# Kernel tuning notes

Hardware: AMD Instinct MI355X
Metric: run time of the kernel (lower is better)

Reference implementation:

```python
import jax, jax.numpy as jnp
import numpy as np

N, E, F_IN, HID, HEADS, OUT = 50000, 600000, 128, 128, 8, 64
C = HID // HEADS  # per-head channels = 16
NEG_SLOPE = 0.2


def _gat_layer(x, ei_src, ei_dst, Wl, bl, Ws, Wd, a_s, a_d, bc):
    n = x.shape[0]
    lin_out = x @ Wl + bl                              # [N, HID]
    xs = (x @ Ws).reshape(n, HEADS, C)                 # [N, H, C] (lin_src, no bias)
    xd = (x @ Wd).reshape(n, HEADS, C)                 # [N, H, C] (lin_dst, no bias)
    alpha_s = jnp.sum(xs * a_s, axis=-1)               # [N, H]
    alpha_d = jnp.sum(xd * a_d, axis=-1)               # [N, H]
    e = jax.nn.leaky_relu(alpha_s[ei_src] + alpha_d[ei_dst], NEG_SLOPE)  # [E, H]
    # segment softmax over destination nodes
    m = jax.lax.stop_gradient(jax.ops.segment_max(e, ei_dst, num_segments=n))
    p = jnp.exp(e - m[ei_dst])
    denom = jax.ops.segment_sum(p, ei_dst, num_segments=n)
    alpha = p / (denom[ei_dst] + 1e-16)                # [E, H]
    msg = alpha[:, :, None] * xs[ei_src]               # [E, H, C]
    agg = jax.ops.segment_sum(msg, ei_dst, num_segments=n).reshape(n, HID) + bc
    # eval mode: attention/feature dropout are identity
    return jax.nn.elu(lin_out + agg)


def setup_inputs() -> dict:
    key = jax.random.key(0)
    ks = jax.random.split(key, 20)
    s = 0.05
    d = {
        "x": jax.random.normal(ks[0], (N, F_IN), jnp.float32),
        "edge_index": jax.random.randint(ks[1], (2, E), 0, N, jnp.int64)
        if jax.config.jax_enable_x64 else jax.random.randint(ks[1], (2, E), 0, N, jnp.int32),
    }
    dims_in = [F_IN, HID]
    for l in range(2):
        di = dims_in[l]
        d[f"W_lin{l}"] = jax.random.normal(ks[2 + 8 * l], (di, HID), jnp.float32) * s
        d[f"b_lin{l}"] = jnp.zeros((HID,), jnp.float32)
        d[f"W_src{l}"] = jax.random.normal(ks[3 + 8 * l], (di, HID), jnp.float32) * s
        d[f"W_dst{l}"] = jax.random.normal(ks[4 + 8 * l], (di, HID), jnp.float32) * s
        d[f"att_src{l}"] = jax.random.normal(ks[5 + 8 * l], (HEADS, C), jnp.float32) * s
        d[f"att_dst{l}"] = jax.random.normal(ks[6 + 8 * l], (HEADS, C), jnp.float32) * s
        d[f"b_conv{l}"] = jnp.zeros((HID,), jnp.float32)
    d["W_out"] = jax.random.normal(ks[18], (HID, OUT), jnp.float32) * s
    d["b_out"] = jnp.zeros((OUT,), jnp.float32)
    return d


def reference(x, edge_index,
              W_lin0, b_lin0, W_src0, W_dst0, att_src0, att_dst0, b_conv0,
              W_lin1, b_lin1, W_src1, W_dst1, att_src1, att_dst1, b_conv1,
              W_out, b_out):
    ei_src, ei_dst = edge_index[0], edge_index[1]
    h = _gat_layer(x, ei_src, ei_dst, W_lin0, b_lin0, W_src0, W_dst0, att_src0, att_dst0, b_conv0)
    h = _gat_layer(h, ei_src, ei_dst, W_lin1, b_lin1, W_src1, W_dst1, att_src1, att_dst1, b_conv1)
    return h @ W_out + b_out
```

## Files before the change

kernel.cpp:

```cpp
#include <hip/hip_runtime.h>
#include <cstdint>
#include <cstddef>

#define NEG_SLOPE 0.2f

typedef __bf16 bf16x8 __attribute__((ext_vector_type(8)));
typedef float f32x4 __attribute__((ext_vector_type(4)));

static __device__ __forceinline__ unsigned short f2bf(float f) {
  unsigned int u = __float_as_uint(f);
  unsigned int r = (u + 0x7FFFu + ((u >> 16) & 1u)) >> 16;
  return (unsigned short)r;
}
static __device__ __forceinline__ float bf2f(unsigned short u) {
  return __uint_as_float(((unsigned int)u) << 16);
}
static __device__ __forceinline__ float pklo(unsigned int x) {
  return __uint_as_float(x << 16);
}
static __device__ __forceinline__ float pkhi(unsigned int x) {
  return __uint_as_float(x & 0xffff0000u);
}

__global__ __launch_bounds__(256) void k_scan_local(const int* __restrict__ deg,
                                                    int* __restrict__ lex,
                                                    int* __restrict__ bsum, int n) {
  __shared__ int ts[256];
  const int t = threadIdx.x;
  const int base = blockIdx.x * 1024 + t * 4;
  int4 d = {0, 0, 0, 0};
  if (base + 3 < n) d = *reinterpret_cast<const int4*>(&deg[base]);
  else {
    if (base + 0 < n) d.x = deg[base + 0];
    if (base + 1 < n) d.y = deg[base + 1];
    if (base + 2 < n) d.z = deg[base + 2];
  }
  int s = d.x + d.y + d.z + d.w;
  ts[t] = s;
  __syncthreads();
  for (int off = 1; off < 256; off <<= 1) {
    int y = (t >= off) ? ts[t - off] : 0;
    __syncthreads();
    ts[t] += y;
    __syncthreads();
  }
  int pre = ts[t] - s;
  int4 o;
  o.x = pre; o.y = pre + d.x; o.z = pre + d.x + d.y; o.w = pre + d.x + d.y + d.z;
  if (base + 3 < n) *reinterpret_cast<int4*>(&lex[base]) = o;
  else {
    if (base + 0 < n) lex[base + 0] = o.x;
    if (base + 1 < n) lex[base + 1] = o.y;
    if (base + 2 < n) lex[base + 2] = o.z;
  }
  if (t == 255) bsum[blockIdx.x] = ts[255];
}

__global__ __launch_bounds__(256) void k_scan_bsum(int* __restrict__ bsum, int nb) {
  __shared__ int ts[256];
  const int t = threadIdx.x;
  int v = (t < nb) ? bsum[t] : 0;
  ts[t] = v;
  __syncthreads();
  for (int off = 1; off < 256; off <<= 1) {
    int y = (t >= off) ? ts[t - off] : 0;
    __syncthreads();
    ts[t] += y;
    __syncthreads();
  }
  if (t < nb) bsum[t] = ts[t] - v;
}

__global__ void k_scan_add(const int* __restrict__ lex, const int* __restrict__ bsum,
                           int* __restrict__ rowptr, int* __restrict__ cursor,
                           int n, int E) {
  int i = blockIdx.x * 256 + threadIdx.x;
  if (i < n) {
    int v = lex[i] + bsum[i >> 10];
    rowptr[i] = v;
    cursor[i] = v;
  }
  if (i == n) rowptr[n] = E;
}

static __device__ __forceinline__ unsigned short pack_wt_elem(
    const float* __restrict__ Wl, const float* __restrict__ Ws,
    const float* __restrict__ Wd, const float* __restrict__ as_,
    const float* __restrict__ ad_, int t) {
  int j = t >> 7, k = t & 127;
  float val;
  if (j < 128) val = Wl[k * 128 + j];
  else if (j < 256) val = Ws[k * 128 + (j - 128)];
  else {
    int jj = j - 256;
    int h = jj & 7;
    const float* W = (jj < 8) ? Ws : Wd;
    const float* a = (jj < 8) ? as_ : ad_;
    float s = 0.f;
#pragma unroll
    for (int c = 0; c < 16; ++c) s += W[k * 128 + h * 16 + c] * a[h * 16 + c];
    val = s;
  }
  return f2bf(val);
}

__global__ void k_init(
    const float* __restrict__ Wl0, const float* __restrict__ Ws0, const float* __restrict__ Wd0,
    const float* __restrict__ as0, const float* __restrict__ ad0,
    const float* __restrict__ Wl1, const float* __restrict__ Ws1, const float* __restrict__ Wd1,
    const float* __restrict__ as1, const float* __restrict__ ad1,
    const float* __restrict__ Wo,
    unsigned short* __restrict__ wt0, unsigned short* __restrict__ wt1,
    unsigned short* __restrict__ wot,
    const int* __restrict__ ei, int* __restrict__ deg, int E, int packBlocks) {
  const int SZ = 272 * 128;
  if ((int)blockIdx.x < packBlocks) {
    int t = blockIdx.x * 256 + threadIdx.x;
    if (t < SZ) {
      wt0[t] = pack_wt_elem(Wl0, Ws0, Wd0, as0, ad0, t);
    } else if (t < 2 * SZ) {
      wt1[t - SZ] = pack_wt_elem(Wl1, Ws1, Wd1, as1, ad1, t - SZ);
    } else if (t < 2 * SZ + 64 * 128) {
      int u = t - 2 * SZ;
      int nn = u >> 7, k = u & 127;
      wot[u] = f2bf(Wo[k * 64 + nn]);
    }
  } else {
    int e = (blockIdx.x - packBlocks) * 256 + threadIdx.x;
    if (e < E) atomicAdd(&deg[ei[E + e]], 1);
  }
}

__global__ __launch_bounds__(256, 3) void k_gemm0_scatter(
    const float* __restrict__ X, const unsigned short* __restrict__ wt,
    const float* __restrict__ bl, const float* __restrict__ bc,
    unsigned int* __restrict__ ylin_pk, unsigned short* __restrict__ xsb,
    unsigned short* __restrict__ asd_s, unsigned short* __restrict__ asd_d,
    int n, int gemmBlocks,
    const int* __restrict__ ei, int* __restrict__ cursor,
    unsigned short* __restrict__ col, int E, int total) {
  __shared__ __align__(16) unsigned short xa[32][136];
  const int i = blockIdx.x;
  const int before = (int)(((long long)i * gemmBlocks) / total);
  const int after  = (int)(((long long)(i + 1) * gemmBlocks) / total);

  if (after == before) {
    int e = (i - after) * 256 + threadIdx.x;
    if (e < E) {
      int d = ei[E + e];
      int pos = atomicAdd(&cursor[d], 1);
      col[pos] = (unsigned short)ei[e];
    }
    return;
  }

  const int tid = threadIdx.x;
  const int wave = tid >> 6, lane = tid & 63;
  const int lr = lane & 15, lg = lane >> 4;
  const int row0 = before * 32;
  const int f0 = wave * 4;
  const bool w3 = (wave == 3);

  bf16x8 bfr[4][4];
#pragma unroll
  for (int ff = 0; ff < 4; ++ff)
#pragma unroll
    for (int s = 0; s < 4; ++s)
      bfr[ff][s] = *reinterpret_cast<const bf16x8*>(
          &wt[(size_t)((f0 + ff) * 16 + lr) * 128 + s * 32 + lg * 8]);
  bf16x8 bfr4[4];
  if (w3) {
#pragma unroll
    for (int s = 0; s < 4; ++s)
      bfr4[s] = *reinterpret_cast<const bf16x8*>(
          &wt[(size_t)(256 + lr) * 128 + s * 32 + lg * 8]);
  }

#pragma unroll
  for (int ii = 0; ii < 4; ++ii) {
    int c = tid + ii * 256;
    int r = c >> 5, kq = c & 31;
    float4 v = make_float4(0.f, 0.f, 0.f, 0.f);
    if (row0 + r < n)
      v = reinterpret_cast<const float4*>(X)[(size_t)(row0 + r) * 32 + kq];
    ushort4 o;
    o.x = f2bf(v.x); o.y = f2bf(v.y); o.z = f2bf(v.z); o.w = f2bf(v.w);
    *reinterpret_cast<ushort4*>(&xa[r][kq * 4]) = o;
  }
  __syncthreads();

  f32x4 acc[2][4];
  f32x4 acc4[2];
#pragma unroll
  for (int g = 0; g < 2; ++g) {
    acc4[g] = (f32x4){0.f, 0.f, 0.f, 0.f};
#pragma unroll
    for (int ff = 0; ff < 4; ++ff) acc[g][ff] = (f32x4){0.f, 0.f, 0.f, 0.f};
  }

#pragma unroll
  for (int s = 0; s < 4; ++s) {
    bf16x8 a0 = *reinterpret_cast<const bf16x8*>(&xa[lr][s * 32 + lg * 8]);
    bf16x8 a1 = *reinterpret_cast<const bf16x8*>(&xa[16 + lr][s * 32 + lg * 8]);
#pragma unroll
    for (int ff = 0; ff < 4; ++ff) {
      acc[0][ff] = __builtin_amdgcn_mfma_f32_16x16x32_bf16(a0, bfr[ff][s], acc[0][ff], 0, 0, 0);
      acc[1][ff] = __builtin_amdgcn_mfma_f32_16x16x32_bf16(a1, bfr[ff][s], acc[1][ff], 0, 0, 0);
    }
    if (w3) {
      acc4[0] = __builtin_amdgcn_mfma_f32_16x16x32_bf16(a0, bfr4[s], acc4[0], 0, 0, 0);
      acc4[1] = __builtin_amdgcn_mfma_f32_16x16x32_bf16(a1, bfr4[s], acc4[1], 0, 0, 0);
    }
  }

  if (f0 < 8) {
#pragma unroll
    for (int g = 0; g < 2; ++g)
#pragma unroll
      for (int ff = 0; ff < 4; ++ff) {
        int j = (f0 + ff) * 16 + lr;
        float blc = bl[j] + bc[j];
#pragma unroll
        for (int r = 0; r < 4; ++r) {
          int row = row0 + g * 16 + lg * 4 + r;
          float vb = acc[g][ff][r] + blc;
          float v2 = __shfl(vb, lane ^ 1);
          if (row < n && (lr & 1) == 0)
            ylin_pk[(size_t)row * 64 + (j >> 1)] =
                (unsigned int)f2bf(vb) | ((unsigned int)f2bf(v2) << 16);
        }
      }
  } else {
#pragma unroll
    for (int g = 0; g < 2; ++g)
#pragma unroll
      for (int ff = 0; ff < 4; ++ff) {
        int j = (f0 - 8 + ff) * 16 + lr;
#pragma unroll
        for (int r = 0; r < 4; ++r) {
          int row = row0 + g * 16 + lg * 4 + r;
          if (row < n) xsb[(size_t)row * 128 + j] = f2bf(acc[g][ff][r]);
        }
      }
    if (w3) {
#pragma unroll
      for (int g = 0; g < 2; ++g)
#pragma unroll
        for (int r = 0; r < 4; ++r) {
          int row = row0 + g * 16 + lg * 4 + r;
          if (row < n) {
            unsigned short v = f2bf(acc4[g][r]);
            if (lr < 8) asd_s[(size_t)row * 8 + lr] = v;
            else        asd_d[(size_t)row * 8 + (lr - 8)] = v;
          }
        }
    }
  }
}

__global__ __launch_bounds__(256, 3) void k_gemm_fused1(
    const unsigned short* __restrict__ X, const unsigned short* __restrict__ wt,
    const float* __restrict__ bl, const float* __restrict__ bc,
    unsigned int* __restrict__ ylin_pk, unsigned short* __restrict__ xsb,
    unsigned short* __restrict__ asd_s, unsigned short* __restrict__ asd_d,
    int n) {
  __shared__ __align__(16) unsigned short xa[32][136];
  const int tid = threadIdx.x;
  const int wave = tid >> 6, lane = tid & 63;
  const int lr = lane & 15, lg = lane >> 4;
  const int row0 = blockIdx.x * 32;
  const int f0 = wave * 4;
  const bool w3 = (wave == 3);

  bf16x8 bfr[4][4];
#pragma unroll
  for (int ff = 0; ff < 4; ++ff)
#pragma unroll
    for (int s = 0; s < 4; ++s)
      bfr[ff][s] = *reinterpret_cast<const bf16x8*>(
          &wt[(size_t)((f0 + ff) * 16 + lr) * 128 + s * 32 + lg * 8]);
  bf16x8 bfr4[4];
  if (w3) {
#pragma unroll
    for (int s = 0; s < 4; ++s)
      bfr4[s] = *reinterpret_cast<const bf16x8*>(
          &wt[(size_t)(256 + lr) * 128 + s * 32 + lg * 8]);
  }

#pragma unroll
  for (int i = 0; i < 2; ++i) {
    int c = tid + i * 256;
    int r = c >> 4, ko = c & 15;
    uint4 v = {0u, 0u, 0u, 0u};
    if (row0 + r < n)
      v = reinterpret_cast<const uint4*>(X)[(size_t)(row0 + r) * 16 + ko];
    *reinterpret_cast<uint4*>(&xa[r][ko * 8]) = v;
  }
  __syncthreads();

  f32x4 acc[2][4];
  f32x4 acc4[2];
#pragma unroll
  for (int g = 0; g < 2; ++g) {
    acc4[g] = (f32x4){0.f, 0.f, 0.f, 0.f};
#pragma unroll
    for (int ff = 0; ff < 4; ++ff) acc[g][ff] = (f32x4){0.f, 0.f, 0.f, 0.f};
  }

#pragma unroll
  for (int s = 0; s < 4; ++s) {
    bf16x8 a0 = *reinterpret_cast<const bf16x8*>(&xa[lr][s * 32 + lg * 8]);
    bf16x8 a1 = *reinterpret_cast<const bf16x8*>(&xa[16 + lr][s * 32 + lg * 8]);
#pragma unroll
    for (int ff = 0; ff < 4; ++ff) {
      acc[0][ff] = __builtin_amdgcn_mfma_f32_16x16x32_bf16(a0, bfr[ff][s], acc[0][ff], 0, 0, 0);
      acc[1][ff] = __builtin_amdgcn_mfma_f32_16x16x32_bf16(a1, bfr[ff][s], acc[1][ff], 0, 0, 0);
    }
    if (w3) {
      acc4[0] = __builtin_amdgcn_mfma_f32_16x16x32_bf16(a0, bfr4[s], acc4[0], 0, 0, 0);
      acc4[1] = __builtin_amdgcn_mfma_f32_16x16x32_bf16(a1, bfr4[s], acc4[1], 0, 0, 0);
    }
  }

  if (f0 < 8) {
#pragma unroll
    for (int g = 0; g < 2; ++g)
#pragma unroll
      for (int ff = 0; ff < 4; ++ff) {
        int j = (f0 + ff) * 16 + lr;
        float blc = bl[j] + bc[j];
#pragma unroll
        for (int r = 0; r < 4; ++r) {
          int row = row0 + g * 16 + lg * 4 + r;
          float vb = acc[g][ff][r] + blc;
          float v2 = __shfl(vb, lane ^ 1);
          if (row < n && (lr & 1) == 0)
            ylin_pk[(size_t)row * 64 + (j >> 1)] =
                (unsigned int)f2bf(vb) | ((unsigned int)f2bf(v2) << 16);
        }
      }
  } else {
#pragma unroll
    for (int g = 0; g < 2; ++g)
#pragma unroll
      for (int ff = 0; ff < 4; ++ff) {
        int j = (f0 - 8 + ff) * 16 + lr;
#pragma unroll
        for (int r = 0; r < 4; ++r) {
          int row = row0 + g * 16 + lg * 4 + r;
          if (row < n) xsb[(size_t)row * 128 + j] = f2bf(acc[g][ff][r]);
        }
      }
    if (w3) {
#pragma unroll
      for (int g = 0; g < 2; ++g)
#pragma unroll
        for (int r = 0; r < 4; ++r) {
          int row = row0 + g * 16 + lg * 4 + r;
          if (row < n) {
            unsigned short v = f2bf(acc4[g][r]);
            if (lr < 8) asd_s[(size_t)row * 8 + lr] = v;
            else        asd_d[(size_t)row * 8 + (lr - 8)] = v;
          }
        }
    }
  }
}

__global__ __launch_bounds__(256, 3) void k_gemm_out(
    const unsigned short* __restrict__ X, const unsigned short* __restrict__ wot,
    const float* __restrict__ bias, float* __restrict__ out, int n) {
  __shared__ __align__(16) unsigned short xa[32][136];
  const int tid = threadIdx.x;
  const int wave = tid >> 6, lane = tid & 63;
  const int lr = lane & 15, lg = lane >> 4;
  const int row0 = blockIdx.x * 32;

  bf16x8 bo[4];
#pragma unroll
  for (int s = 0; s < 4; ++s)
    bo[s] = *reinterpret_cast<const bf16x8*>(
        &wot[(size_t)(wave * 16 + lr) * 128 + s * 32 + lg * 8]);

#pragma unroll
  for (int i = 0; i < 2; ++i) {
    int c = tid + i * 256;
    int r = c >> 4, ko = c & 15;
    uint4 v = {0u, 0u, 0u, 0u};
    if (row0 + r < n)
      v = reinterpret_cast<const uint4*>(X)[(size_t)(row0 + r) * 16 + ko];
    *reinterpret_cast<uint4*>(&xa[r][ko * 8]) = v;
  }
  __syncthreads();

  f32x4 acc[2];
  acc[0] = (f32x4){0.f, 0.f, 0.f, 0.f};
  acc[1] = (f32x4){0.f, 0.f, 0.f, 0.f};
#pragma unroll
  for (int s = 0; s < 4; ++s) {
    bf16x8 a0 = *reinterpret_cast<const bf16x8*>(&xa[lr][s * 32 + lg * 8]);
    bf16x8 a1 = *reinterpret_cast<const bf16x8*>(&xa[16 + lr][s * 32 + lg * 8]);
    acc[0] = __builtin_amdgcn_mfma_f32_16x16x32_bf16(a0, bo[s], acc[0], 0, 0, 0);
    acc[1] = __builtin_amdgcn_mfma_f32_16x16x32_bf16(a1, bo[s], acc[1], 0, 0, 0);
  }
  float bv = bias[wave * 16 + lr];
#pragma unroll
  for (int g = 0; g < 2; ++g)
#pragma unroll
    for (int r = 0; r < 4; ++r) {
      int row = row0 + g * 16 + lg * 4 + r;
      if (row < n) out[(size_t)row * 64 + wave * 16 + lr] = acc[g][r] + bv;
    }
}

__global__ __launch_bounds__(256) void k_aggregate(
    const unsigned int* __restrict__ ylin_pk, const unsigned int* __restrict__ xsp,
    const unsigned short* __restrict__ asd_s, const unsigned short* __restrict__ asd_d,
    const int* __restrict__ rowptr, const unsigned short* __restrict__ col,
    unsigned int* __restrict__ hout_pk, int n) {
  int node = (blockIdx.x * blockDim.x + threadIdx.x) >> 6;
  if (node >= n) return;
  const int lane = threadIdx.x & 63;
  const int el = lane >> 3;
  const int hh = lane & 7;
  const int hb4 = (lane >> 3) << 2;
  const int beg = rowptr[node], end = rowptr[node + 1];

  const float ad_hh = bf2f(asd_d[(size_t)node * 8 + hh]);
  unsigned int y = __builtin_nontemporal_load(&ylin_pk[(size_t)node * 64 + lane]);

  float dsum = 0.f, acc0 = 0.f, acc1 = 0.f;
  int ebase = beg;
  for (; ebase + 8 < end; ebase += 16) {
    int eA = ebase + el;
    int eB = ebase + 8 + el;
    bool vB = eB < end;
    int esB = vB ? eB : (end - 1);
    int srcA = (int)__builtin_nontemporal_load(&col[eA]);
    int srcB = (int)__builtin_nontemporal_load(&col[esB]);
    float svA = bf2f(asd_s[(size_t)srcA * 8 + hh]) + ad_hh;
    float svB = bf2f(asd_s[(size_t)srcB * 8 + hh]) + ad_hh;
    svA = fmaxf(svA, NEG_SLOPE * svA);
    svB = fmaxf(svB, NEG_SLOPE * svB);
    float peA = __expf(svA);
    float peB = vB ? __expf(svB) : 0.f;
#pragma unroll
    for (int q = 0; q < 8; ++q) {
      float pq = __uint_as_float(__builtin_amdgcn_ds_bpermute(
          q * 32 + hb4, __float_as_uint(peA)));
      int sq = __builtin_amdgcn_readlane(srcA, q * 8);
      unsigned int xv = xsp[(size_t)sq * 64 + lane];
      dsum += pq;
      acc0 += pq * pklo(xv);
      acc1 += pq * pkhi(xv);
    }
#pragma unroll
    for (int q = 0; q < 8; ++q) {
      float pq = __uint_as_float(__builtin_amdgcn_ds_bpermute(
          q * 32 + hb4, __float_as_uint(peB)));
      int sq = __builtin_amdgcn_readlane(srcB, q * 8);
      unsigned int xv = xsp[(size_t)sq * 64 + lane];
      dsum += pq;
      acc0 += pq * pklo(xv);
      acc1 += pq * pkhi(xv);
    }
  }
  for (; ebase < end; ebase += 8) {
    int e1 = ebase + el;
    bool valid = e1 < end;
    int esafe = valid ? e1 : (end - 1);
    int srcp = (int)__builtin_nontemporal_load(&col[esafe]);
    float sv = bf2f(asd_s[(size_t)srcp * 8 + hh]) + ad_hh;
    sv = fmaxf(sv, NEG_SLOPE * sv);
    float pe = valid ? __expf(sv) : 0.f;
#pragma unroll
    for (int q = 0; q < 8; ++q) {
      float pq = __uint_as_float(__builtin_amdgcn_ds_bpermute(
          q * 32 + hb4, __float_as_uint(pe)));
      int sq = __builtin_amdgcn_readlane(srcp, q * 8);
      unsigned int xv = xsp[(size_t)sq * 64 + lane];
      dsum += pq;
      acc0 += pq * pklo(xv);
      acc1 += pq * pkhi(xv);
    }
  }
  float inv = 1.f / (dsum + 1e-16f);
  float l0 = pklo(y) + acc0 * inv;
  float l1 = pkhi(y) + acc1 * inv;
  l0 = l0 > 0.f ? l0 : __expf(l0) - 1.f;
  l1 = l1 > 0.f ? l1 : __expf(l1) - 1.f;
  hout_pk[(size_t)node * 64 + lane] =
      (unsigned int)f2bf(l0) | ((unsigned int)f2bf(l1) << 16);
}

extern "C" void kernel_launch(void* const* d_in, const int* in_sizes, int n_in,
                              void* d_out, int out_size, void* d_ws, size_t ws_size,
                              hipStream_t stream) {
  const float* x      = (const float*)d_in[0];
  const int*   ei     = (const int*)d_in[1];
  const float* W_lin0 = (const float*)d_in[2];
  const float* b_lin0 = (const float*)d_in[3];
  const float* W_src0 = (const float*)d_in[4];
  const float* W_dst0 = (const float*)d_in[5];
  const float* att_s0 = (const float*)d_in[6];
  const float* att_d0 = (const float*)d_in[7];
  const float* b_cnv0 = (const float*)d_in[8];
  const float* W_lin1 = (const float*)d_in[9];
  const float* b_lin1 = (const float*)d_in[10];
  const float* W_src1 = (const float*)d_in[11];
  const float* W_dst1 = (const float*)d_in[12];
  const float* att_s1 = (const float*)d_in[13];
  const float* att_d1 = (const float*)d_in[14];
  const float* b_cnv1 = (const float*)d_in[15];
  const float* W_out  = (const float*)d_in[16];
  const float* b_out  = (const float*)d_in[17];
  float* out = (float*)d_out;

  const int N = in_sizes[0] / 128;
  const int E = in_sizes[1] / 2;
  const int NB = (N + 1023) / 1024;
  const int MB32 = (N + 31) / 32;
  const int SB = (E + 255) / 256;
  const int PACKB = (2 * 272 * 128 + 64 * 128 + 255) / 256;

  char* p = (char*)d_ws;
  unsigned int* ylin    = (unsigned int*)p;   p += (size_t)N * 64 * 4;
  unsigned short* xsb   = (unsigned short*)p; p += (size_t)N * 128 * 2;
  unsigned short* hb    = (unsigned short*)p; p += (size_t)N * 128 * 2;
  unsigned short* asd_s = (unsigned short*)p; p += (size_t)N * 8 * 2;
  unsigned short* asd_d = (unsigned short*)p; p += (size_t)N * 8 * 2;
  unsigned short* wt0   = (unsigned short*)p; p += (size_t)272 * 128 * 2;
  unsigned short* wt1   = (unsigned short*)p; p += (size_t)272 * 128 * 2;
  unsigned short* wot   = (unsigned short*)p; p += (size_t)64 * 128 * 2;
  int* rowptr = (int*)p;                      p += (size_t)(N + 4) * 4;
  int* cursor = (int*)p;                      p += (size_t)N * 4;
  int* deg    = (int*)p;                      p += (size_t)N * 4;
  int* lex    = (int*)p;                      p += (size_t)N * 4;
  int* bsum   = (int*)p;                      p += (size_t)256 * 4;
  unsigned short* col = (unsigned short*)p;   p += (size_t)E * 2;

  dim3 b256(256);

  hipMemsetAsync(deg, 0, (size_t)N * 4, stream);
  k_init<<<PACKB + SB, b256, 0, stream>>>(
      W_lin0, W_src0, W_dst0, att_s0, att_d0,
      W_lin1, W_src1, W_dst1, att_s1, att_d1,
      W_out, wt0, wt1, wot, ei, deg, E, PACKB);
  k_scan_local<<<NB, b256, 0, stream>>>(deg, lex, bsum, N);
  k_scan_bsum<<<1, b256, 0, stream>>>(bsum, NB);
  k_scan_add<<<(N + 256) / 256, b256, 0, stream>>>(lex, bsum, rowptr, cursor, N, E);

  k_gemm0_scatter<<<MB32 + SB, b256, 0, stream>>>(
      x, wt0, b_lin0, b_cnv0, ylin, xsb, asd_s, asd_d, N, MB32,
      ei, cursor, col, E, MB32 + SB);

  k_aggregate<<<(N + 3) / 4, b256, 0, stream>>>(
      ylin, (const unsigned int*)xsb, asd_s, asd_d, rowptr, col,
      (unsigned int*)hb, N);
  k_gemm_fused1<<<MB32, b256, 0, stream>>>(hb, wt1, b_lin1, b_cnv1,
                                           ylin, xsb, asd_s, asd_d, N);
  k_aggregate<<<(N + 3) / 4, b256, 0, stream>>>(
      ylin, (const unsigned int*)xsb, asd_s, asd_d, rowptr, col,
      (unsigned int*)hb, N);
  k_gemm_out<<<MB32, b256, 0, stream>>>(hb, wot, b_out, out, N);
}
```

Measured before the change: 165.3 us.

## Record edge rank during degree count and merge block-sum scan into add

Result: faster. 157.8 us (-4.6%).

```diff
diff --git a/kernel.cpp b/kernel.cpp
--- a/kernel.cpp
+++ b/kernel.cpp
@@ -56,7 +56,9 @@
   if (t == 255) bsum[blockIdx.x] = ts[255];
 }
 
-__global__ __launch_bounds__(256) void k_scan_bsum(int* __restrict__ bsum, int nb) {
+__global__ __launch_bounds__(256) void k_scan_add(
+    const int* __restrict__ lex, const int* __restrict__ bsum,
+    int* __restrict__ rowptr, int n, int nb, int E) {
   __shared__ int ts[256];
   const int t = threadIdx.x;
   int v = (t < nb) ? bsum[t] : 0;
@@ -68,18 +70,12 @@
     ts[t] += y;
     __syncthreads();
   }
-  if (t < nb) bsum[t] = ts[t] - v;
-}
-
-__global__ void k_scan_add(const int* __restrict__ lex, const int* __restrict__ bsum,
-                           int* __restrict__ rowptr, int* __restrict__ cursor,
-                           int n, int E) {
-  int i = blockIdx.x * 256 + threadIdx.x;
-  if (i < n) {
-    int v = lex[i] + bsum[i >> 10];
-    rowptr[i] = v;
-    cursor[i] = v;
-  }
+  int excl = ts[t] - v;
+  __syncthreads();
+  ts[t] = excl;
+  __syncthreads();
+  int i = blockIdx.x * 256 + t;
+  if (i < n) rowptr[i] = lex[i] + ts[i >> 10];
   if (i == n) rowptr[n] = E;
 }
 
@@ -112,7 +108,8 @@
     const float* __restrict__ Wo,
     unsigned short* __restrict__ wt0, unsigned short* __restrict__ wt1,
     unsigned short* __restrict__ wot,
-    const int* __restrict__ ei, int* __restrict__ deg, int E, int packBlocks) {
+    const int* __restrict__ ei, int* __restrict__ deg,
+    unsigned short* __restrict__ rank, int E, int packBlocks) {
   const int SZ = 272 * 128;
   if ((int)blockIdx.x < packBlocks) {
     int t = blockIdx.x * 256 + threadIdx.x;
@@ -127,7 +124,8 @@
     }
   } else {
     int e = (blockIdx.x - packBlocks) * 256 + threadIdx.x;
-    if (e < E) atomicAdd(&deg[ei[E + e]], 1);
+    if (e < E)
+      rank[e] = (unsigned short)atomicAdd(&deg[ei[E + e]], 1);
   }
 }
 
@@ -137,7 +135,8 @@
     unsigned int* __restrict__ ylin_pk, unsigned short* __restrict__ xsb,
     unsigned short* __restrict__ asd_s, unsigned short* __restrict__ asd_d,
     int n, int gemmBlocks,
-    const int* __restrict__ ei, int* __restrict__ cursor,
+    const int* __restrict__ ei, const int* __restrict__ rowptr,
+    const unsigned short* __restrict__ rank,
     unsigned short* __restrict__ col, int E, int total) {
   __shared__ __align__(16) unsigned short xa[32][136];
   const int i = blockIdx.x;
@@ -148,7 +147,7 @@
     int e = (i - after) * 256 + threadIdx.x;
     if (e < E) {
       int d = ei[E + e];
-      int pos = atomicAdd(&cursor[d], 1);
+      int pos = rowptr[d] + (int)rank[e];
       col[pos] = (unsigned short)ei[e];
     }
     return;
@@ -533,11 +532,11 @@
   unsigned short* wt1   = (unsigned short*)p; p += (size_t)272 * 128 * 2;
   unsigned short* wot   = (unsigned short*)p; p += (size_t)64 * 128 * 2;
   int* rowptr = (int*)p;                      p += (size_t)(N + 4) * 4;
-  int* cursor = (int*)p;                      p += (size_t)N * 4;
   int* deg    = (int*)p;                      p += (size_t)N * 4;
   int* lex    = (int*)p;                      p += (size_t)N * 4;
   int* bsum   = (int*)p;                      p += (size_t)256 * 4;
-  unsigned short* col = (unsigned short*)p;   p += (size_t)E * 2;
+  unsigned short* col  = (unsigned short*)p;  p += (size_t)E * 2;
+  unsigned short* rank = (unsigned short*)p;  p += (size_t)E * 2;
 
   dim3 b256(256);
 
@@ -545,14 +544,13 @@
   k_init<<<PACKB + SB, b256, 0, stream>>>(
       W_lin0, W_src0, W_dst0, att_s0, att_d0,
       W_lin1, W_src1, W_dst1, att_s1, att_d1,
-      W_out, wt0, wt1, wot, ei, deg, E, PACKB);
+      W_out, wt0, wt1, wot, ei, deg, rank, E, PACKB);
   k_scan_local<<<NB, b256, 0, stream>>>(deg, lex, bsum, N);
-  k_scan_bsum<<<1, b256, 0, stream>>>(bsum, NB);
-  k_scan_add<<<(N + 256) / 256, b256, 0, stream>>>(lex, bsum, rowptr, cursor, N, E);
+  k_scan_add<<<(N + 256) / 256, b256, 0, stream>>>(lex, bsum, rowptr, N, NB, E);
 
   k_gemm0_scatter<<<MB32 + SB, b256, 0, stream>>>(
       x, wt0, b_lin0, b_cnv0, ylin, xsb, asd_s, asd_d, N, MB32,
-      ei, cursor, col, E, MB32 + SB);
+      ei, rowptr, rank, col, E, MB32 + SB);
 
   k_aggregate<<<(N + 3) / 4, b256, 0, stream>>>(
       ylin, (const unsigned int*)xsb, asd_s, asd_d, rowptr, col,
```
